# Performance work log

Measured on AMD Instinct MI355X. Metric: run time of the kernel, lower is better.

The kernel has to match this reference:

```python
import jax, jax.numpy as jnp
import numpy as np

B, C, L, E = 65536, 16, 32, 32
EPS = 1e-12

def _normalize(x, axis=-1):
    # F.normalize: x / max(||x||_2, eps)
    n = jnp.sqrt(jnp.sum(x * x, axis=axis, keepdims=True))
    return x / jnp.maximum(n, EPS)

def _linear(x, W, b):
    # torch nn.Linear: y = x @ W.T + b, W: [out, in]
    return jnp.einsum('bcl,el->bce', x, W) + b

def setup_inputs() -> dict:
    key = jax.random.key(0)
    ks = jax.random.split(key, 12)
    s_l = 1.0 / np.sqrt(L)
    s_p1 = 1.0 / np.sqrt(C * E)
    s_p2 = 1.0 / np.sqrt(C * 3)
    return {
        'embed1': jax.random.normal(ks[0], (B, C, L), jnp.float32),
        'embed2': jax.random.normal(ks[1], (B, C, L), jnp.float32),
        'qW': jax.random.uniform(ks[2], (E, L), jnp.float32, -s_l, s_l),
        'qb': jax.random.uniform(ks[3], (E,), jnp.float32, -s_l, s_l),
        'kW': jax.random.uniform(ks[4], (E, L), jnp.float32, -s_l, s_l),
        'kb': jax.random.uniform(ks[5], (E,), jnp.float32, -s_l, s_l),
        'vW': jax.random.uniform(ks[6], (E, L), jnp.float32, -s_l, s_l),
        'vb': jax.random.uniform(ks[7], (E,), jnp.float32, -s_l, s_l),
        'p1W': jax.random.uniform(ks[8], (C * 3, C * E), jnp.float32, -s_p1, s_p1),
        'p1b': jax.random.uniform(ks[9], (C * 3,), jnp.float32, -s_p1, s_p1),
        'p2W': jax.random.uniform(ks[10], (3, C * 3), jnp.float32, -s_p2, s_p2),
        'p2b': jax.random.uniform(ks[11], (3,), jnp.float32, -s_p2, s_p2),
    }

def reference(embed1, embed2, qW, qb, kW, kb, vW, vb, p1W, p1b, p2W, p2b):
    query = _linear(embed1, qW, qb) * _linear(embed2, qW, qb)   # [B,C,E]
    key_t = _linear(embed1, kW, kb) * _linear(embed2, kW, kb)   # [B,C,E]
    value = _linear(embed1, vW, vb) * _linear(embed2, vW, vb)   # [B,C,E]
    attn = jnp.einsum('bce,bde->bcd', _normalize(query), _normalize(key_t))  # [B,C,C]
    # torch F.softmax with dim=None on a 3-D tensor -> legacy dim=0 (batch axis)
    attn = jax.nn.softmax(attn, axis=0)
    # dropout(p=0.2) is identity in eval mode
    out = jnp.einsum('bcd,bce->bde', attn, value)  # attn.transpose(1,2) @ value, [B,C,E]
    h = out.reshape(out.shape[0], -1)              # [B, C*E]
    h = jax.nn.relu(h @ p1W.T + p1b) @ p2W.T + p2b  # [B, 3]
    return _normalize(h)
```

## Files before the change

kernel.cpp:

```cpp
#include <hip/hip_runtime.h>

#define B_TOT 65536
#define WS_P1W 4096
#define WS_EV  (1u << 20)
#define EV_BYTES 100663296u
#define WS_PART (WS_EV + EV_BYTES)

typedef float f32x4 __attribute__((ext_vector_type(4)));
typedef short s16x8 __attribute__((ext_vector_type(8)));

__device__ __forceinline__ float bf2f(unsigned short h) {
    unsigned u = ((unsigned)h) << 16;
    return __builtin_bit_cast(float, u);
}
__device__ __forceinline__ unsigned pack2(float a, float b) {
    unsigned ua = __builtin_bit_cast(unsigned, a) + 0x8000u;
    unsigned ub = __builtin_bit_cast(unsigned, b) + 0x8000u;
    return __builtin_amdgcn_perm(ub, ua, 0x07060302u);
}
__device__ __forceinline__ unsigned short f2bf(float f) {
    return (unsigned short)((__builtin_bit_cast(unsigned, f) + 0x8000u) >> 16);
}
__device__ __forceinline__ s16x8 cvt8(float4 a, float4 b) {
    uint4 u;
    u.x = pack2(a.x, a.y); u.y = pack2(a.z, a.w);
    u.z = pack2(b.x, b.y); u.w = pack2(b.z, b.w);
    return __builtin_bit_cast(s16x8, u);
}
#define MFMA(a, b, c) __builtin_amdgcn_mfma_f32_16x16x32_bf16((a), (b), (c), 0, 0, 0)

__global__ __launch_bounds__(256) void k1_stats(
    const float* __restrict__ e1, const float* __restrict__ e2,
    const float* __restrict__ qW, const float* __restrict__ qb,
    const float* __restrict__ kW, const float* __restrict__ kb,
    const float* __restrict__ vW, const float* __restrict__ vb,
    char* __restrict__ ws, int blkoff) {

    const int tid = threadIdx.x;
    const int lane = tid & 63;
    const int widx = tid >> 6;
    const int col = lane & 15;
    const int quad = lane >> 4;

    __shared__ __align__(16) unsigned short qk_lds[4][2][2][16 * 40];
    __shared__ float Dblk[256];
    if (blkoff == 0 && blockIdx.x == 0) ((float*)ws)[tid] = 0.f;
    Dblk[tid] = 0.f;
    __syncthreads();

    s16x8 wq[2], wk[2], wv[2];
    float bq[2], bk[2], bv[2];
#pragma unroll
    for (int h = 0; h < 2; ++h) {
        int row = col + 16 * h;
        const float4* pq = (const float4*)(qW + row * 32 + quad * 8);
        const float4* pk = (const float4*)(kW + row * 32 + quad * 8);
        const float4* pv = (const float4*)(vW + row * 32 + quad * 8);
        wq[h] = cvt8(pq[0], pq[1]);
        wk[h] = cvt8(pk[0], pk[1]);
        wv[h] = cvt8(pv[0], pv[1]);
        bq[h] = qb[row]; bk[h] = kb[row]; bv[h] = vb[row];
    }

    float dacc[4] = {0.f, 0.f, 0.f, 0.f};
    char* evbase = ws + WS_EV;
    const f32x4 z = {0.f, 0.f, 0.f, 0.f};

    const int gw = (blkoff + blockIdx.x) * 4 + widx;
    for (int i = 0; i < 4; ++i) {
        s16x8 fx1[2], fx2[2];
#pragma unroll
        for (int p = 0; p < 2; ++p) {
            const int b = gw * 8 + i * 2 + p;
            const float4* x1p = (const float4*)(e1 + (size_t)b * 512 + col * 32 + quad * 8);
            const float4* x2p = (const float4*)(e2 + (size_t)b * 512 + col * 32 + quad * 8);
            float4 a0 = x1p[0], a1 = x1p[1];
            float4 b0 = x2p[0], b1 = x2p[1];
            fx1[p] = cvt8(a0, a1);
            fx2[p] = cvt8(b0, b1);
        }
#pragma unroll
        for (int p = 0; p < 2; ++p) {
            const int b = gw * 8 + i * 2 + p;
            char* bbase = evbase + (size_t)b * 1536;
            {
                f32x4 qa = MFMA(fx1[p], wq[0], z), qc = MFMA(fx2[p], wq[0], z);
                f32x4 qd = MFMA(fx1[p], wq[1], z), qe = MFMA(fx2[p], wq[1], z);
                unsigned* dst = (unsigned*)qk_lds[widx][0][p];
#pragma unroll
                for (int r = 0; r < 4; ++r)
                    dst[(quad * 4 + r) * 20 + col] =
                        pack2((qa[r] + bq[0]) * (qc[r] + bq[0]),
                              (qd[r] + bq[1]) * (qe[r] + bq[1]));
            }
            {
                f32x4 ka = MFMA(fx1[p], wk[0], z), kc = MFMA(fx2[p], wk[0], z);
                f32x4 kd = MFMA(fx1[p], wk[1], z), ke = MFMA(fx2[p], wk[1], z);
                unsigned* dst = (unsigned*)qk_lds[widx][1][p];
#pragma unroll
                for (int r = 0; r < 4; ++r)
                    dst[(quad * 4 + r) * 20 + col] =
                        pack2((ka[r] + bk[0]) * (kc[r] + bk[0]),
                              (kd[r] + bk[1]) * (ke[r] + bk[1]));
            }
            {
                f32x4 va = MFMA(fx1[p], wv[0], z), vc = MFMA(fx2[p], wv[0], z);
                f32x4 vd = MFMA(fx1[p], wv[1], z), ve = MFMA(fx2[p], wv[1], z);
                uint2 vst0, vst1;
                vst0.x = pack2((va[0] + bv[0]) * (vc[0] + bv[0]),
                               (va[1] + bv[0]) * (vc[1] + bv[0]));
                vst0.y = pack2((va[2] + bv[0]) * (vc[2] + bv[0]),
                               (va[3] + bv[0]) * (vc[3] + bv[0]));
                vst1.x = pack2((vd[0] + bv[1]) * (ve[0] + bv[1]),
                               (vd[1] + bv[1]) * (ve[1] + bv[1]));
                vst1.y = pack2((vd[2] + bv[1]) * (ve[2] + bv[1]),
                               (vd[3] + bv[1]) * (ve[3] + bv[1]));
                *(uint2*)(bbase + 512 + ((0 * 16 + col) * 2 + (quad >> 1)) * 16 + (quad & 1) * 8) = vst0;
                *(uint2*)(bbase + 512 + ((1 * 16 + col) * 2 + (quad >> 1)) * 16 + (quad & 1) * 8) = vst1;
            }
        }
#pragma unroll
        for (int p = 0; p < 2; ++p) {
            const int b = gw * 8 + i * 2 + p;
            char* bbase = evbase + (size_t)b * 1536;
            const unsigned short* qbuf = qk_lds[widx][0][p];
            const unsigned short* kbuf = qk_lds[widx][1][p];
            s16x8 aq  = *(const s16x8*)(qbuf + col * 40 + quad * 8);
            s16x8 bk8 = *(const s16x8*)(kbuf + col * 40 + quad * 8);
            f32x4 S = MFMA(aq, bk8, z);

            float ssq = 0.f, ssk = 0.f;
#pragma unroll
            for (int j = 0; j < 8; ++j) {
                float qf = bf2f((unsigned short)aq[j]);  ssq += qf * qf;
                float kf = bf2f((unsigned short)bk8[j]); ssk += kf * kf;
            }
            ssq += __shfl_xor(ssq, 16); ssq += __shfl_xor(ssq, 32);
            ssk += __shfl_xor(ssk, 16); ssk += __shfl_xor(ssk, 32);
            float invq = 1.f / fmaxf(sqrtf(ssq), 1e-12f);
            float invk = 1.f / fmaxf(sqrtf(ssk), 1e-12f);
            float iq0 = __shfl(invq, quad * 4 + 0);
            float iq1 = __shfl(invq, quad * 4 + 1);
            float iq2 = __shfl(invq, quad * 4 + 2);
            float iq3 = __shfl(invq, quad * 4 + 3);

            float ex0 = __expf(S[0] * (iq0 * invk));
            float ex1 = __expf(S[1] * (iq1 * invk));
            float ex2 = __expf(S[2] * (iq2 * invk));
            float ex3 = __expf(S[3] * (iq3 * invk));
            dacc[0] += ex0; dacc[1] += ex1; dacc[2] += ex2; dacc[3] += ex3;
            uint2 est; est.x = pack2(ex0, ex1); est.y = pack2(ex2, ex3);
            *(uint2*)(bbase + col * 32 + quad * 8) = est;
        }
    }
#pragma unroll
    for (int r = 0; r < 4; ++r)
        atomicAdd(&Dblk[col * 16 + quad * 4 + r], dacc[r]);
    __syncthreads();
    ((float*)(ws + WS_PART))[(size_t)(blkoff + blockIdx.x) * 256 + tid] = Dblk[tid];
}

__global__ __launch_bounds__(256) void k1b_prep(const float* __restrict__ p1W,
                                                char* __restrict__ ws) {
    const int t = threadIdx.x;
    const int g = blockIdx.x;
    const int idx = g * 256 + t;
    {
        int jj   = idx & 7;
        int lane = (idx >> 3) & 63;
        int ktnt = idx >> 9;
        int kt = ktnt & 15, nt = ktnt >> 4;
        int n_lo = lane & 15, q8 = lane >> 4;
        int j2  = nt * 16 + n_lo;
        int ip  = kt * 32 + q8 * 8 + jj;
        int e_lo = ip >> 5, qq = (ip >> 3) & 3, hh = (ip >> 2) & 1, r = ip & 3;
        int orig = (qq * 4 + r) * 32 + (e_lo + 16 * hh);
        ((unsigned short*)(ws + WS_P1W))[idx] = f2bf(p1W[j2 * 512 + orig]);
    }
    if (g < 16) {
        const float* part = (const float*)(ws + WS_PART);
        float s = 0.f;
        for (int r = 0; r < 128; ++r)
            s += part[(size_t)(g * 128 + r) * 256 + t];
        atomicAdd(((float*)ws) + t, s);
    }
}

__global__ __launch_bounds__(256) void k2_apply(
    const char* __restrict__ ws, const float* __restrict__ p1b,
    const float* __restrict__ p2W, const float* __restrict__ p2b,
    float* __restrict__ out) {

    const int tid = threadIdx.x;
    const int lane = tid & 63;
    const int widx = tid >> 6;
    const int col = lane & 15;
    const int quad = lane >> 4;
    const int qm = quad & 1;

    __shared__ __align__(16) unsigned short Hs[16 * 512];
    float* P = (float*)Hs;

    float p1bias[3], p2w[3][3];
#pragma unroll
    for (int nt = 0; nt < 3; ++nt) {
        p1bias[nt] = p1b[col + 16 * nt];
#pragma unroll
        for (int t2 = 0; t2 < 3; ++t2) p2w[nt][t2] = p2W[t2 * 48 + col + 16 * nt];
    }
    const float pb0 = p2b[0], pb1 = p2b[1], pb2 = p2b[2];

    const float* Dws = (const float*)ws;
    const float4 dva = *(const float4*)(Dws + col * 16 + qm * 8);
    const float4 dvb = *(const float4*)(Dws + col * 16 + qm * 8 + 4);
    float dinv[8] = {1.f / dva.x, 1.f / dva.y, 1.f / dva.z, 1.f / dva.w,
                     1.f / dvb.x, 1.f / dvb.y, 1.f / dvb.z, 1.f / dvb.w};

    const char* evbase = ws + WS_EV;
    const unsigned short* p1wp = (const unsigned short*)(ws + WS_P1W);
    const int g = blockIdx.x;
    const f32x4 z = {0.f, 0.f, 0.f, 0.f};
    const s16x8 zz = {0, 0, 0, 0, 0, 0, 0, 0};

    {
        const char* bb0 = evbase + (size_t)(g * 16 + widx * 4) * 1536;
        const int eoff  = col * 32 + qm * 16;
        const int voff0 = 512 + (col * 2 + qm) * 16;
        const int voff1 = 512 + ((16 + col) * 2 + qm) * 16;
        s16x8 ne  = *(const s16x8*)(bb0 + eoff);
        s16x8 nv0 = *(const s16x8*)(bb0 + voff0);
        s16x8 nv1 = *(const s16x8*)(bb0 + voff1);
#pragma unroll
        for (int ii = 0; ii < 4; ++ii) {
            s16x8 eraw = ne, bf0 = nv0, bf1 = nv1;
            if (ii < 3) {
                const char* nb = bb0 + (size_t)(ii + 1) * 1536;
                ne  = *(const s16x8*)(nb + eoff);
                nv0 = *(const s16x8*)(nb + voff0);
                nv1 = *(const s16x8*)(nb + voff1);
            }
            float ef[8];
#pragma unroll
            for (int j = 0; j < 8; ++j)
                ef[j] = bf2f((unsigned short)eraw[j]) * dinv[j];
            uint4 ua;
            ua.x = pack2(ef[0], ef[1]); ua.y = pack2(ef[2], ef[3]);
            ua.z = pack2(ef[4], ef[5]); ua.w = pack2(ef[6], ef[7]);
            s16x8 afrag = __builtin_bit_cast(s16x8, ua);
            if (quad >= 2) { afrag = zz; bf0 = zz; bf1 = zz; }
            f32x4 o0 = MFMA(afrag, bf0, z);
            f32x4 o1 = MFMA(afrag, bf1, z);
            uint4 uh;
            uh.x = pack2(o0[0], o0[1]); uh.y = pack2(o0[2], o0[3]);
            uh.z = pack2(o1[0], o1[1]); uh.w = pack2(o1[2], o1[3]);
            const int i = widx * 4 + ii;
            int chunk = (col * 4 + quad) ^ (i & 7);
            *(uint4*)(Hs + i * 512 + chunk * 8) = uh;
        }
    }
    __syncthreads();

    f32x4 acc[3] = {z, z, z};
    {
        const int kt0 = widx * 4;
        s16x8 nw0 = *(const s16x8*)(p1wp + ((0 * 16 + kt0) * 64 + lane) * 8);
        s16x8 nw1 = *(const s16x8*)(p1wp + ((1 * 16 + kt0) * 64 + lane) * 8);
        s16x8 nw2 = *(const s16x8*)(p1wp + ((2 * 16 + kt0) * 64 + lane) * 8);
#pragma unroll
        for (int t2 = 0; t2 < 4; ++t2) {
            const int kt = widx * 4 + t2;
            s16x8 w0 = nw0, w1 = nw1, w2 = nw2;
            if (t2 < 3) {
                nw0 = *(const s16x8*)(p1wp + ((0 * 16 + kt + 1) * 64 + lane) * 8);
                nw1 = *(const s16x8*)(p1wp + ((1 * 16 + kt + 1) * 64 + lane) * 8);
                nw2 = *(const s16x8*)(p1wp + ((2 * 16 + kt + 1) * 64 + lane) * 8);
            }
            int chunk = (kt * 4 + quad) ^ (col & 7);
            s16x8 a = *(const s16x8*)(Hs + col * 512 + chunk * 8);
            acc[0] = MFMA(a, w0, acc[0]);
            acc[1] = MFMA(a, w1, acc[1]);
            acc[2] = MFMA(a, w2, acc[2]);
        }
    }
    __syncthreads();

#pragma unroll
    for (int nt = 0; nt < 3; ++nt)
        *(f32x4*)(P + (widx * 64 + lane) * 12 + nt * 4) = acc[nt];
    __syncthreads();

    {
        float s3[3] = {0.f, 0.f, 0.f};
#pragma unroll
        for (int w = 0; w < 4; ++w)
#pragma unroll
            for (int nt = 0; nt < 3; ++nt)
                s3[nt] += P[(w * 64 + lane) * 12 + nt * 4 + widx];
        float pp[3] = {0.f, 0.f, 0.f};
#pragma unroll
        for (int nt = 0; nt < 3; ++nt) {
            float hv = fmaxf(s3[nt] + p1bias[nt], 0.f);
            pp[0] += hv * p2w[nt][0];
            pp[1] += hv * p2w[nt][1];
            pp[2] += hv * p2w[nt][2];
        }
#pragma unroll
        for (int m = 1; m <= 8; m <<= 1) {
            pp[0] += __shfl_xor(pp[0], m);
            pp[1] += __shfl_xor(pp[1], m);
            pp[2] += __shfl_xor(pp[2], m);
        }
        float h0 = pp[0] + pb0, h1 = pp[1] + pb1, h2 = pp[2] + pb2;
        float inv = 1.f / fmaxf(sqrtf(h0 * h0 + h1 * h1 + h2 * h2), 1e-12f);
        if (col < 3) {
            float v = (col == 0) ? h0 : ((col == 1) ? h1 : h2);
            out[(size_t)(g * 16 + quad * 4 + widx) * 3 + col] = v * inv;
        }
    }
}

extern "C" void kernel_launch(void* const* d_in, const int* in_sizes, int n_in,
                              void* d_out, int out_size, void* d_ws, size_t ws_size,
                              hipStream_t stream) {
    const float* e1  = (const float*)d_in[0];
    const float* e2  = (const float*)d_in[1];
    const float* qW  = (const float*)d_in[2];
    const float* qb  = (const float*)d_in[3];
    const float* kW  = (const float*)d_in[4];
    const float* kb  = (const float*)d_in[5];
    const float* vW  = (const float*)d_in[6];
    const float* vb  = (const float*)d_in[7];
    const float* p1W = (const float*)d_in[8];
    const float* p1b = (const float*)d_in[9];
    const float* p2W = (const float*)d_in[10];
    const float* p2b = (const float*)d_in[11];
    float* out = (float*)d_out;
    char* ws = (char*)d_ws;

    k1_stats<<<1024, 256, 0, stream>>>(e1, e2, qW, qb, kW, kb, vW, vb, ws, 0);
    k1_stats<<<1024, 256, 0, stream>>>(e1, e2, qW, qb, kW, kb, vW, vb, ws, 1024);
    k1b_prep<<<96, 256, 0, stream>>>(p1W, ws);
    k2_apply<<<4096, 256, 0, stream>>>(ws, p1b, p2W, p2b, out);
}
```

Measured before the change: 352.6 us.

## Process one batch per wave in k1 with a single large launch

```diff
diff --git a/kernel.cpp b/kernel.cpp
--- a/kernel.cpp
+++ b/kernel.cpp
@@ -34,7 +34,7 @@
     const float* __restrict__ qW, const float* __restrict__ qb,
     const float* __restrict__ kW, const float* __restrict__ kb,
     const float* __restrict__ vW, const float* __restrict__ vb,
-    char* __restrict__ ws, int blkoff) {
+    char* __restrict__ ws) {
 
     const int tid = threadIdx.x;
     const int lane = tid & 63;
@@ -42,9 +42,9 @@
     const int col = lane & 15;
     const int quad = lane >> 4;
 
-    __shared__ __align__(16) unsigned short qk_lds[4][2][2][16 * 40];
+    __shared__ __align__(16) unsigned short qk_lds[4][2][16 * 40];
     __shared__ float Dblk[256];
-    if (blkoff == 0 && blockIdx.x == 0) ((float*)ws)[tid] = 0.f;
+    if (blockIdx.x == 0) ((float*)ws)[tid] = 0.f;
     Dblk[tid] = 0.f;
     __syncthreads();
 
@@ -62,102 +62,88 @@
         bq[h] = qb[row]; bk[h] = kb[row]; bv[h] = vb[row];
     }
 
-    float dacc[4] = {0.f, 0.f, 0.f, 0.f};
     char* evbase = ws + WS_EV;
     const f32x4 z = {0.f, 0.f, 0.f, 0.f};
 
-    const int gw = (blkoff + blockIdx.x) * 4 + widx;
-    for (int i = 0; i < 4; ++i) {
-        s16x8 fx1[2], fx2[2];
-#pragma unroll
-        for (int p = 0; p < 2; ++p) {
-            const int b = gw * 8 + i * 2 + p;
-            const float4* x1p = (const float4*)(e1 + (size_t)b * 512 + col * 32 + quad * 8);
-            const float4* x2p = (const float4*)(e2 + (size_t)b * 512 + col * 32 + quad * 8);
-            float4 a0 = x1p[0], a1 = x1p[1];
-            float4 b0 = x2p[0], b1 = x2p[1];
-            fx1[p] = cvt8(a0, a1);
-            fx2[p] = cvt8(b0, b1);
-        }
-#pragma unroll
-        for (int p = 0; p < 2; ++p) {
-            const int b = gw * 8 + i * 2 + p;
-            char* bbase = evbase + (size_t)b * 1536;
-            {
-                f32x4 qa = MFMA(fx1[p], wq[0], z), qc = MFMA(fx2[p], wq[0], z);
-                f32x4 qd = MFMA(fx1[p], wq[1], z), qe = MFMA(fx2[p], wq[1], z);
-                unsigned* dst = (unsigned*)qk_lds[widx][0][p];
-#pragma unroll
-                for (int r = 0; r < 4; ++r)
-                    dst[(quad * 4 + r) * 20 + col] =
-                        pack2((qa[r] + bq[0]) * (qc[r] + bq[0]),
-                              (qd[r] + bq[1]) * (qe[r] + bq[1]));
-            }
-            {
-                f32x4 ka = MFMA(fx1[p], wk[0], z), kc = MFMA(fx2[p], wk[0], z);
-                f32x4 kd = MFMA(fx1[p], wk[1], z), ke = MFMA(fx2[p], wk[1], z);
-                unsigned* dst = (unsigned*)qk_lds[widx][1][p];
-#pragma unroll
-                for (int r = 0; r < 4; ++r)
-                    dst[(quad * 4 + r) * 20 + col] =
-                        pack2((ka[r] + bk[0]) * (kc[r] + bk[0]),
-                              (kd[r] + bk[1]) * (ke[r] + bk[1]));
-            }
-            {
-                f32x4 va = MFMA(fx1[p], wv[0], z), vc = MFMA(fx2[p], wv[0], z);
-                f32x4 vd = MFMA(fx1[p], wv[1], z), ve = MFMA(fx2[p], wv[1], z);
-                uint2 vst0, vst1;
-                vst0.x = pack2((va[0] + bv[0]) * (vc[0] + bv[0]),
-                               (va[1] + bv[0]) * (vc[1] + bv[0]));
-                vst0.y = pack2((va[2] + bv[0]) * (vc[2] + bv[0]),
-                               (va[3] + bv[0]) * (vc[3] + bv[0]));
-                vst1.x = pack2((vd[0] + bv[1]) * (ve[0] + bv[1]),
-                               (vd[1] + bv[1]) * (ve[1] + bv[1]));
-                vst1.y = pack2((vd[2] + bv[1]) * (ve[2] + bv[1]),
-                               (vd[3] + bv[1]) * (ve[3] + bv[1]));
-                *(uint2*)(bbase + 512 + ((0 * 16 + col) * 2 + (quad >> 1)) * 16 + (quad & 1) * 8) = vst0;
-                *(uint2*)(bbase + 512 + ((1 * 16 + col) * 2 + (quad >> 1)) * 16 + (quad & 1) * 8) = vst1;
-            }
-        }
-#pragma unroll
-        for (int p = 0; p < 2; ++p) {
-            const int b = gw * 8 + i * 2 + p;
-            char* bbase = evbase + (size_t)b * 1536;
-            const unsigned short* qbuf = qk_lds[widx][0][p];
-            const unsigned short* kbuf = qk_lds[widx][1][p];
-            s16x8 aq  = *(const s16x8*)(qbuf + col * 40 + quad * 8);
-            s16x8 bk8 = *(const s16x8*)(kbuf + col * 40 + quad * 8);
-            f32x4 S = MFMA(aq, bk8, z);
-
-            float ssq = 0.f, ssk = 0.f;
-#pragma unroll
-            for (int j = 0; j < 8; ++j) {
-                float qf = bf2f((unsigned short)aq[j]);  ssq += qf * qf;
-                float kf = bf2f((unsigned short)bk8[j]); ssk += kf * kf;
-            }
-            ssq += __shfl_xor(ssq, 16); ssq += __shfl_xor(ssq, 32);
-            ssk += __shfl_xor(ssk, 16); ssk += __shfl_xor(ssk, 32);
-            float invq = 1.f / fmaxf(sqrtf(ssq), 1e-12f);
-            float invk = 1.f / fmaxf(sqrtf(ssk), 1e-12f);
-            float iq0 = __shfl(invq, quad * 4 + 0);
-            float iq1 = __shfl(invq, quad * 4 + 1);
-            float iq2 = __shfl(invq, quad * 4 + 2);
-            float iq3 = __shfl(invq, quad * 4 + 3);
-
-            float ex0 = __expf(S[0] * (iq0 * invk));
-            float ex1 = __expf(S[1] * (iq1 * invk));
-            float ex2 = __expf(S[2] * (iq2 * invk));
-            float ex3 = __expf(S[3] * (iq3 * invk));
-            dacc[0] += ex0; dacc[1] += ex1; dacc[2] += ex2; dacc[3] += ex3;
-            uint2 est; est.x = pack2(ex0, ex1); est.y = pack2(ex2, ex3);
-            *(uint2*)(bbase + col * 32 + quad * 8) = est;
-        }
-    }
-#pragma unroll
-    for (int r = 0; r < 4; ++r)
-        atomicAdd(&Dblk[col * 16 + quad * 4 + r], dacc[r]);
-    __syncthreads();
-    ((float*)(ws + WS_PART))[(size_t)(blkoff + blockIdx.x) * 256 + tid] = Dblk[tid];
+    const int b = blockIdx.x * 4 + widx;
+    const float4* x1p = (const float4*)(e1 + (size_t)b * 512 + col * 32 + quad * 8);
+    const float4* x2p = (const float4*)(e2 + (size_t)b * 512 + col * 32 + quad * 8);
+    float4 a0 = x1p[0], a1 = x1p[1];
+    float4 b0 = x2p[0], b1 = x2p[1];
+    s16x8 fx1 = cvt8(a0, a1);
+    s16x8 fx2 = cvt8(b0, b1);
+
+    char* bbase = evbase + (size_t)b * 1536;
+    {
+        f32x4 qa = MFMA(fx1, wq[0], z), qc = MFMA(fx2, wq[0], z);
+        f32x4 qd = MFMA(fx1, wq[1], z), qe = MFMA(fx2, wq[1], z);
+        unsigned* dst = (unsigned*)qk_lds[widx][0];
+#pragma unroll
+        for (int r = 0; r < 4; ++r)
+            dst[(quad * 4 + r) * 20 + col] =
+                pack2((qa[r] + bq[0]) * (qc[r] + bq[0]),
+                      (qd[r] + bq[1]) * (qe[r] + bq[1]));
+    }
+    {
+        f32x4 ka = MFMA(fx1, wk[0], z), kc = MFMA(fx2, wk[0], z);
+        f32x4 kd = MFMA(fx1, wk[1], z), ke = MFMA(fx2, wk[1], z);
+        unsigned* dst = (unsigned*)qk_lds[widx][1];
+#pragma unroll
+        for (int r = 0; r < 4; ++r)
+            dst[(quad * 4 + r) * 20 + col] =
+                pack2((ka[r] + bk[0]) * (kc[r] + bk[0]),
+                      (kd[r] + bk[1]) * (ke[r] + bk[1]));
+    }
+    {
+        f32x4 va = MFMA(fx1, wv[0], z), vc = MFMA(fx2, wv[0], z);
+        f32x4 vd = MFMA(fx1, wv[1], z), ve = MFMA(fx2, wv[1], z);
+        uint2 vst0, vst1;
+        vst0.x = pack2((va[0] + bv[0]) * (vc[0] + bv[0]),
+                       (va[1] + bv[0]) * (vc[1] + bv[0]));
+        vst0.y = pack2((va[2] + bv[0]) * (vc[2] + bv[0]),
+                       (va[3] + bv[0]) * (vc[3] + bv[0]));
+        vst1.x = pack2((vd[0] + bv[1]) * (ve[0] + bv[1]),
+                       (vd[1] + bv[1]) * (ve[1] + bv[1]));
+        vst1.y = pack2((vd[2] + bv[1]) * (ve[2] + bv[1]),
+                       (vd[3] + bv[1]) * (ve[3] + bv[1]));
+        *(uint2*)(bbase + 512 + ((0 * 16 + col) * 2 + (quad >> 1)) * 16 + (quad & 1) * 8) = vst0;
+        *(uint2*)(bbase + 512 + ((1 * 16 + col) * 2 + (quad >> 1)) * 16 + (quad & 1) * 8) = vst1;
+    }
+
+    const unsigned short* qbuf = qk_lds[widx][0];
+    const unsigned short* kbuf = qk_lds[widx][1];
+    s16x8 aq  = *(const s16x8*)(qbuf + col * 40 + quad * 8);
+    s16x8 bk8 = *(const s16x8*)(kbuf + col * 40 + quad * 8);
+    f32x4 S = MFMA(aq, bk8, z);
+
+    float ssq = 0.f, ssk = 0.f;
+#pragma unroll
+    for (int j = 0; j < 8; ++j) {
+        float qf = bf2f((unsigned short)aq[j]);  ssq += qf * qf;
+        float kf = bf2f((unsigned short)bk8[j]); ssk += kf * kf;
+    }
+    ssq += __shfl_xor(ssq, 16); ssq += __shfl_xor(ssq, 32);
+    ssk += __shfl_xor(ssk, 16); ssk += __shfl_xor(ssk, 32);
+    float invq = 1.f / fmaxf(sqrtf(ssq), 1e-12f);
+    float invk = 1.f / fmaxf(sqrtf(ssk), 1e-12f);
+    float iq0 = __shfl(invq, quad * 4 + 0);
+    float iq1 = __shfl(invq, quad * 4 + 1);
+    float iq2 = __shfl(invq, quad * 4 + 2);
+    float iq3 = __shfl(invq, quad * 4 + 3);
+
+    float ex0 = __expf(S[0] * (iq0 * invk));
+    float ex1 = __expf(S[1] * (iq1 * invk));
+    float ex2 = __expf(S[2] * (iq2 * invk));
+    float ex3 = __expf(S[3] * (iq3 * invk));
+    uint2 est; est.x = pack2(ex0, ex1); est.y = pack2(ex2, ex3);
+    *(uint2*)(bbase + col * 32 + quad * 8) = est;
+
+    atomicAdd(&Dblk[col * 16 + quad * 4 + 0], ex0);
+    atomicAdd(&Dblk[col * 16 + quad * 4 + 1], ex1);
+    atomicAdd(&Dblk[col * 16 + quad * 4 + 2], ex2);
+    atomicAdd(&Dblk[col * 16 + quad * 4 + 3], ex3);
+    __syncthreads();
+    ((float*)(ws + WS_PART))[(size_t)blockIdx.x * 256 + tid] = Dblk[tid];
 }
 
 __global__ __launch_bounds__(256) void k1b_prep(const float* __restrict__ p1W,
@@ -180,8 +166,9 @@
     if (g < 16) {
         const float* part = (const float*)(ws + WS_PART);
         float s = 0.f;
-        for (int r = 0; r < 128; ++r)
-            s += part[(size_t)(g * 128 + r) * 256 + t];
+#pragma unroll 8
+        for (int r = 0; r < 1024; ++r)
+            s += part[(size_t)(g * 1024 + r) * 256 + t];
         atomicAdd(((float*)ws) + t, s);
     }
 }
@@ -337,8 +324,7 @@
     float* out = (float*)d_out;
     char* ws = (char*)d_ws;
 
-    k1_stats<<<1024, 256, 0, stream>>>(e1, e2, qW, qb, kW, kb, vW, vb, ws, 0);
-    k1_stats<<<1024, 256, 0, stream>>>(e1, e2, qW, qb, kW, kb, vW, vb, ws, 1024);
+    k1_stats<<<16384, 256, 0, stream>>>(e1, e2, qW, qb, kW, kb, vW, vb, ws);
     k1b_prep<<<96, 256, 0, stream>>>(p1W, ws);
     k2_apply<<<4096, 256, 0, stream>>>(ws, p1b, p2W, p2b, out);
 }
```

Measured after the change: 418.4 us. 18.7% more time.
